# Optimization experiments

Measured on AMD Instinct MI355X. Metric: run time of the kernel, lower is better.

## Reference

```python
import jax, jax.numpy as jnp
import numpy as np

N, E, IN, H, OUT, G = 50000, 800000, 128, 256, 10, 512


def setup_inputs() -> dict:
    key = jax.random.key(0)
    ks = jax.random.split(key, 12)
    def lin(k, fan_in, fan_out):
        s = 1.0 / np.sqrt(fan_in)
        kw, kb = jax.random.split(k)
        W = jax.random.uniform(kw, (fan_in, fan_out), jnp.float32, -s, s)
        b = jax.random.uniform(kb, (fan_out,), jnp.float32, -s, s)
        return W, b
    x = jax.random.normal(ks[0], (N, IN), jnp.float32)
    edge_index = jax.random.randint(ks[1], (2, E), 0, N)
    batch = jnp.sort(jax.random.randint(ks[2], (N,), 0, G))
    W1a, b1a = lin(ks[3], IN, H)
    W1b, b1b = lin(ks[4], H, H)
    W2a, b2a = lin(ks[5], H, H)
    W2b, b2b = lin(ks[6], H, H)
    Wlin, blin = lin(ks[7], H, OUT)
    eps1 = jnp.zeros((), jnp.float32)
    eps2 = jnp.zeros((), jnp.float32)
    return dict(x=x, edge_index=edge_index, batch=batch,
                eps1=eps1, W1a=W1a, b1a=b1a, W1b=W1b, b1b=b1b,
                eps2=eps2, W2a=W2a, b2a=b2a, W2b=W2b, b2b=b2b,
                Wlin=Wlin, blin=blin)


def reference(x, edge_index, batch, eps1, W1a, b1a, W1b, b1b,
              eps2, W2a, b2a, W2b, b2b, Wlin, blin):
    src, dst = edge_index[0], edge_index[1]
    # GINConv 1: h = MLP((1+eps)*x + sum_{j in N(i)} x_j)
    agg = jax.ops.segment_sum(x[src], dst, num_segments=N)  # [N, IN]
    h = (1.0 + eps1) * x + agg
    h = jax.nn.relu(h @ W1a + b1a) @ W1b + b1b              # [N, H]
    h = jax.nn.relu(h)  # (dropout p=0.3 is identity in eval mode)
    # GINConv 2
    agg2 = jax.ops.segment_sum(h[src], dst, num_segments=N)  # [N, H]
    h2 = (1.0 + eps2) * h + agg2
    h2 = jax.nn.relu(h2 @ W2a + b2a) @ W2b + b2b             # [N, H]
    # global mean pool per graph
    psum = jax.ops.segment_sum(h2, batch, num_segments=G)    # [G, H]
    cnt = jax.ops.segment_sum(jnp.ones((N, 1), h2.dtype), batch, num_segments=G)
    pooled = psum / jnp.maximum(cnt, 1.0)
    out = pooled @ Wlin + blin                               # [G, OUT]
    return jax.nn.log_softmax(out, axis=-1)
```

## Files before the change

kernel.cpp:

```cpp
#include <hip/hip_runtime.h>
#include <math.h>
#include <stdint.h>

constexpr int N   = 50000;
constexpr int E   = 800000;
constexpr int IN  = 128;
constexpr int H   = 256;
constexpr int OUT = 10;
constexpr int G   = 512;
constexpr int BSTR = 64;

constexpr int NPART  = 391;
constexpr int SEGCAP = 48;
constexpr int EPB    = 4096;
constexpr int AB     = (E + EPB - 1) / EPB;

typedef __bf16 bf16x8 __attribute__((ext_vector_type(8)));
typedef float  f32x4  __attribute__((ext_vector_type(4)));
typedef float  f32x2  __attribute__((ext_vector_type(2)));

__device__ __forceinline__ float blo(unsigned v) { return __uint_as_float(v << 16); }
__device__ __forceinline__ float bhi(unsigned v) { return __uint_as_float(v & 0xffff0000u); }
__device__ __forceinline__ unsigned short f2b(float f) {
  unsigned u = __float_as_uint(f);
  u += 0x7fffu + ((u >> 16) & 1u);
  return (unsigned short)(u >> 16);
}
__device__ __forceinline__ unsigned packb(float lo, float hi) {
  return (unsigned)f2b(lo) | ((unsigned)f2b(hi) << 16);
}
__device__ __forceinline__ unsigned pk_fp8x4(float a, float b, float c, float d) {
  int r = 0;
  r = __builtin_amdgcn_cvt_pk_fp8_f32(a, b, r, false);
  r = __builtin_amdgcn_cvt_pk_fp8_f32(c, d, r, true);
  return (unsigned)r;
}
__device__ __forceinline__ unsigned char fp8_1(float v) {
  return (unsigned char)(__builtin_amdgcn_cvt_pk_fp8_f32(v, v, 0, false) & 0xff);
}


constexpr int XQ_BLOCKS  = (N * IN / 4) / 256;
constexpr int W1A_BLOCKS = (256 * IN) / 256;
constexpr int WH_BLOCKS  = (256 * H) / 256;

__global__ __launch_bounds__(256) void prep_kernel(
    const int* __restrict__ srcp, const int* __restrict__ dstp,
    unsigned* __restrict__ pbuf, int* __restrict__ pcnt,
    const float* __restrict__ x, unsigned* __restrict__ xq,
    const float* __restrict__ W1a, unsigned short* __restrict__ Wt1a,
    const float* __restrict__ W1b, unsigned short* __restrict__ Wt1b,
    const float* __restrict__ W2a, unsigned short* __restrict__ Wt2a,
    const float* __restrict__ W2b, unsigned short* __restrict__ Wt2b) {
  __shared__ int lcur[NPART];
  int b = blockIdx.x;
  int t = threadIdx.x;
  if (b < AB) {
    for (int j = t; j < NPART; j += 256) lcur[j] = 0;
    __syncthreads();
    const int e0 = b * EPB;
#pragma unroll
    for (int r = 0; r < EPB / 1024; ++r) {
      int base = e0 + (r * 256 + t) * 4;
      if (base < E) {
        int4 d4 = *(const int4*)(dstp + base);
        int4 s4 = *(const int4*)(srcp + base);
        int dd[4] = {d4.x, d4.y, d4.z, d4.w};
        int ss[4] = {s4.x, s4.y, s4.z, s4.w};
#pragma unroll
        for (int u = 0; u < 4; ++u) {
          int part = dd[u] >> 7, dl = dd[u] & 127;
          int pos = atomicAdd(&lcur[part], 1);
          if (pos < SEGCAP)
            pbuf[((size_t)part * AB + b) * SEGCAP + pos] =
                ((unsigned)dl << 16) | (unsigned)ss[u];
        }
      }
    }
    __syncthreads();
    for (int j = t; j < NPART; j += 256) pcnt[b * NPART + j] = min(lcur[j], SEGCAP);
    return;
  }
  b -= AB;
  if (b < XQ_BLOCKS) {
    int id = b * 256 + t;
    float4 v = ((const float4*)x)[id];
    xq[id] = pk_fp8x4(v.x, v.y, v.z, v.w);
    return;
  }
  b -= XQ_BLOCKS;
  if (b < W1A_BLOCKS) {
    int id = b * 256 + t;
    int n = id >> 7, k = id & 127;
    Wt1a[id] = f2b(W1a[k * 256 + n]);
    return;
  }
  b -= W1A_BLOCKS;
  const float* Ws;
  unsigned short* Wd;
  if (b < WH_BLOCKS)            { Ws = W1b; Wd = Wt1b; }
  else if (b < 2 * WH_BLOCKS)   { Ws = W2a; Wd = Wt2a; b -= WH_BLOCKS; }
  else                          { Ws = W2b; Wd = Wt2b; b -= 2 * WH_BLOCKS; }
  int id = b * 256 + t;
  int n = id >> 8, k = id & 255;
  Wd[id] = f2b(Ws[k * 256 + n]);
}


__global__ __launch_bounds__(256) void csr_kernel(const unsigned* __restrict__ pbuf,
                                                  const int* __restrict__ pcnt,
                                                  int* __restrict__ deg, int* __restrict__ csre) {
  __shared__ int sa[256], sb[256];
  __shared__ int ldeg[128];
  int p = blockIdx.x;
  int t = threadIdx.x;
  if (t < 128) ldeg[t] = 0;
  sa[t] = (t < AB) ? pcnt[t * NPART + p] : 0;
  __syncthreads();
  int* cur = sa; int* nxt = sb;
#pragma unroll
  for (int off = 1; off < 256; off <<= 1) {
    nxt[t] = cur[t] + ((t >= off) ? cur[t - off] : 0);
    __syncthreads();
    int* tmp = cur; cur = nxt; nxt = tmp;
  }
  int T = cur[255];
  const unsigned* seg = pbuf + (size_t)p * AB * SEGCAP;
  for (int f = t; f < T; f += 256) {
    int lo = 0, hi = AB - 1;
    while (lo < hi) { int m = (lo + hi) >> 1; if (cur[m] > f) hi = m; else lo = m + 1; }
    int bb = lo;
    int excl = bb ? cur[bb - 1] : 0;
    unsigned v = seg[(size_t)bb * SEGCAP + (f - excl)];
    int dl = (int)(v >> 16), s = (int)(v & 0xFFFFu);
    int pos = atomicAdd(&ldeg[dl], 1);
    if (pos < BSTR) csre[(((size_t)p << 7) + dl) * BSTR + pos] = s;
  }
  __syncthreads();
  if (t < 128) {
    int node = (p << 7) + t;
    if (node < N) deg[node] = min(ldeg[t], BSTR);
  }
}


template <int RS>
__global__ __launch_bounds__(64) void agg_pair_kernel(
    const unsigned char* __restrict__ inq,
    const int* __restrict__ deg, const int* __restrict__ csre,
    const float* __restrict__ epsp, unsigned short* __restrict__ out) {
  constexpr int NPAIR = N / 2;
  int bx = blockIdx.x;
  int half = (RS == 256) ? (bx / NPAIR) : 0;
  int pair = (RS == 256) ? (bx - half * NPAIR) : bx;
  int lane = threadIdx.x;
  int hsel = lane >> 5;
  int l = lane & 31;
  int i = pair * 2 + hsel;
  int dg = deg[i]; if (dg > BSTR) dg = BSTR;
  const int* bkt = csre + (size_t)i * BSTR;
  int dgmax = max(dg, __shfl_xor(dg, 32));
  const unsigned char* rowbase = inq + half * 128 + l * 4;
  float a0 = 0.f, a1 = 0.f, a2 = 0.f, a3 = 0.f;
  int hi_j = dg - 1; if (hi_j < 0) hi_j = 0;
  for (int j = 0; j < dgmax; j += 8) {
    unsigned idx[8], v[8];
#pragma unroll
    for (int u = 0; u < 8; ++u) {
      int jc = j + u; if (jc > hi_j) jc = hi_j;
      unsigned raw = (unsigned)bkt[jc];
      idx[u] = raw < (unsigned)N ? raw : 0u;
    }
#pragma unroll
    for (int u = 0; u < 8; ++u) v[u] = *(const unsigned*)(rowbase + (size_t)idx[u] * RS);
#pragma unroll
    for (int u = 0; u < 8; ++u) {
      float s = (j + u < dg) ? 1.f : 0.f;
      f32x2 lo = __builtin_amdgcn_cvt_pk_f32_fp8((int)v[u], false);
      f32x2 hh = __builtin_amdgcn_cvt_pk_f32_fp8((int)v[u], true);
      a0 += s * lo.x; a1 += s * lo.y; a2 += s * hh.x; a3 += s * hh.y;
    }
  }
  float sc = 1.0f + epsp[0];
  unsigned sv = *(const unsigned*)(rowbase + (size_t)i * RS);
  f32x2 slo = __builtin_amdgcn_cvt_pk_f32_fp8((int)sv, false);
  f32x2 shi = __builtin_amdgcn_cvt_pk_f32_fp8((int)sv, true);
  a0 += sc * slo.x; a1 += sc * slo.y; a2 += sc * shi.x; a3 += sc * shi.y;
  unsigned short* orow = out + (size_t)i * RS + half * 128 + l * 4;
  *(uint2*)orow = make_uint2(packb(a0, a1), packb(a2, a3));
}


template <int K, bool RELU, bool OUT8>
__global__ __launch_bounds__(256, 2) void gemm_bf16_kernel(const unsigned short* __restrict__ A,
                                                           const unsigned short* __restrict__ Bt,
                                                           const float* __restrict__ bias,
                                                           void* __restrict__ outv,
                                                           int Nrows) {
  constexpr int M = 256, LDK = 40;
  __shared__ __align__(16) unsigned short As[128 * LDK];
  __shared__ __align__(16) unsigned short Bs[256 * LDK];
  const int tid  = threadIdx.x;
  const int r0   = blockIdx.x * 128;
  const int wave = tid >> 6, lane = tid & 63;
  const int quad = lane >> 4, l15 = lane & 15;
  const int wrow = (wave >> 1) * 64, wcol = (wave & 1) * 64;
  const int srow = tid >> 2;
  const int sk8  = (tid & 3) * 8;

  f32x4 acc[2][4][4];
#pragma unroll
  for (int c = 0; c < 2; ++c)
#pragma unroll
    for (int i = 0; i < 4; ++i)
#pragma unroll
      for (int j = 0; j < 4; ++j) acc[c][i][j] = (f32x4){0.f, 0.f, 0.f, 0.f};

  for (int k0 = 0; k0 < K; k0 += 32) {
    {
      int grow = r0 + srow;
      uint4 v = make_uint4(0u, 0u, 0u, 0u);
      if (grow < Nrows) v = *(const uint4*)(A + (size_t)grow * K + k0 + sk8);
      *(uint4*)(As + srow * LDK + sk8) = v;
      grow = r0 + srow + 64;
      uint4 w = make_uint4(0u, 0u, 0u, 0u);
      if (grow < Nrows) w = *(const uint4*)(A + (size_t)grow * K + k0 + sk8);
      *(uint4*)(As + (srow + 64) * LDK + sk8) = w;
#pragma unroll
      for (int sgm = 0; sgm < 4; ++sgm) {
        int col = srow + sgm * 64;
        *(uint4*)(Bs + col * LDK + sk8) = *(const uint4*)(Bt + (size_t)col * K + k0 + sk8);
      }
    }
    __syncthreads();
    bf16x8 af[4];
#pragma unroll
    for (int mt = 0; mt < 4; ++mt)
      af[mt] = *(const bf16x8*)(As + (wrow + mt * 16 + l15) * LDK + quad * 8);
#pragma unroll
    for (int ch = 0; ch < 2; ++ch) {
      bf16x8 bfr[4];
#pragma unroll
      for (int nt = 0; nt < 4; ++nt)
        bfr[nt] = *(const bf16x8*)(Bs + (ch * 128 + wcol + nt * 16 + l15) * LDK + quad * 8);
#pragma unroll
      for (int mt = 0; mt < 4; ++mt)
#pragma unroll
        for (int nt = 0; nt < 4; ++nt)
          acc[ch][mt][nt] =
              __builtin_amdgcn_mfma_f32_16x16x32_bf16(af[mt], bfr[nt], acc[ch][mt][nt], 0, 0, 0);
    }
    __syncthreads();
  }

#pragma unroll
  for (int ch = 0; ch < 2; ++ch) {
    float bv[4];
#pragma unroll
    for (int nt = 0; nt < 4; ++nt) bv[nt] = bias[ch * 128 + wcol + nt * 16 + l15];
#pragma unroll
    for (int mt = 0; mt < 4; ++mt) {
      int gr0 = r0 + wrow + mt * 16 + quad * 4;
#pragma unroll
      for (int i = 0; i < 4; ++i) {
        int grow = gr0 + i;
        if (grow >= Nrows) continue;
#pragma unroll
        for (int nt = 0; nt < 4; ++nt) {
          float v = acc[ch][mt][nt][i] + bv[nt];
          if (RELU) v = fmaxf(v, 0.f);
          int col = ch * 128 + wcol + nt * 16 + l15;
          if (OUT8) ((unsigned char*)outv)[(size_t)grow * M + col] = fp8_1(v);
          else      ((unsigned short*)outv)[(size_t)grow * M + col] = f2b(v);
        }
      }
    }
  }
}


__global__ __launch_bounds__(128) void pool_final_kernel(const unsigned short* __restrict__ h2,
                                                         const int* __restrict__ batch,
                                                         const float* __restrict__ Wlin,
                                                         const float* __restrict__ blin,
                                                         float* __restrict__ out) {
  __shared__ float sp[H];
  __shared__ float logits[OUT];
  int g = blockIdx.x;
  int t = threadIdx.x;
  int lo = 0, hi = N;
  while (lo < hi) { int m = (lo + hi) >> 1; if (batch[m] < g) lo = m + 1; else hi = m; }
  int s = lo;
  lo = 0; hi = N;
  while (lo < hi) { int m = (lo + hi) >> 1; if (batch[m] < g + 1) lo = m + 1; else hi = m; }
  int e = lo;
  float a0 = 0.f, a1 = 0.f;
  const unsigned* base = (const unsigned*)h2;
  int n = s;
  for (; n + 4 <= e; n += 4) {
    unsigned v0 = base[(size_t)(n + 0) * (H / 2) + t];
    unsigned v1 = base[(size_t)(n + 1) * (H / 2) + t];
    unsigned v2 = base[(size_t)(n + 2) * (H / 2) + t];
    unsigned v3 = base[(size_t)(n + 3) * (H / 2) + t];
    a0 += blo(v0) + blo(v1) + blo(v2) + blo(v3);
    a1 += bhi(v0) + bhi(v1) + bhi(v2) + bhi(v3);
  }
  for (; n < e; ++n) {
    unsigned v = base[(size_t)n * (H / 2) + t];
    a0 += blo(v); a1 += bhi(v);
  }
  float inv = 1.0f / fmaxf((float)(e - s), 1.0f);
  sp[2 * t]     = a0 * inv;
  sp[2 * t + 1] = a1 * inv;
  __syncthreads();
  if (t < OUT) {
    float acc = blin[t];
    for (int k = 0; k < H; ++k) acc = fmaf(sp[k], Wlin[k * OUT + t], acc);
    logits[t] = acc;
  }
  __syncthreads();
  if (t == 0) {
    float m = -INFINITY;
    for (int j = 0; j < OUT; ++j) m = fmaxf(m, logits[j]);
    float ssum = 0.f;
    for (int j = 0; j < OUT; ++j) ssum += expf(logits[j] - m);
    float ls = logf(ssum);
    for (int j = 0; j < OUT; ++j) out[(size_t)g * OUT + j] = logits[j] - m - ls;
  }
}


static inline char* align_up(char* p, size_t a) {
  return (char*)(((uintptr_t)p + a - 1) & ~(a - 1));
}

extern "C" void kernel_launch(void* const* d_in, const int* in_sizes, int n_in,
                              void* d_out, int out_size, void* d_ws, size_t ws_size,
                              hipStream_t stream) {
  const float* x    = (const float*)d_in[0];
  const int*   ei   = (const int*)d_in[1];
  const int*   srcp = ei;
  const int*   dstp = ei + E;
  const int*   batch = (const int*)d_in[2];
  const float* eps1 = (const float*)d_in[3];
  const float* W1a  = (const float*)d_in[4];
  const float* b1a  = (const float*)d_in[5];
  const float* W1b  = (const float*)d_in[6];
  const float* b1b  = (const float*)d_in[7];
  const float* eps2 = (const float*)d_in[8];
  const float* W2a  = (const float*)d_in[9];
  const float* b2a  = (const float*)d_in[10];
  const float* W2b  = (const float*)d_in[11];
  const float* b2b  = (const float*)d_in[12];
  const float* Wlin = (const float*)d_in[13];
  const float* blin = (const float*)d_in[14];
  float* outp = (float*)d_out;

  char* p = (char*)d_ws;
  unsigned* pbuf = (unsigned*)p;     p = align_up(p + (size_t)NPART * AB * SEGCAP * 4, 256);
  int* pcnt = (int*)p;               p = align_up(p + (size_t)AB * NPART * 4, 256);
  int* deg  = (int*)p;               p = align_up(p + (size_t)N * 4, 256);
  int* csre = (int*)p;               p = align_up(p + (size_t)NPART * 128 * BSTR * 4, 256);
  unsigned* xq = (unsigned*)p;       p = align_up(p + (size_t)N * IN, 256);
  unsigned char* h1q = (unsigned char*)p;  p = align_up(p + (size_t)N * H, 256);
  unsigned short* B1 = (unsigned short*)p; p = align_up(p + (size_t)N * IN * 2, 256);
  unsigned short* B2 = (unsigned short*)p; p = align_up(p + (size_t)N * H * 2, 256);
  unsigned short* B3 = (unsigned short*)p; p = align_up(p + (size_t)N * H * 2, 256);
  unsigned short* Wt1a = (unsigned short*)p;  p = align_up(p + (size_t)H * IN * 2, 256);
  unsigned short* Wt1b = (unsigned short*)p;  p = align_up(p + (size_t)H * H * 2, 256);
  unsigned short* Wt2a = (unsigned short*)p;  p = align_up(p + (size_t)H * H * 2, 256);
  unsigned short* Wt2b = (unsigned short*)p;  p = align_up(p + (size_t)H * H * 2, 256);

  prep_kernel<<<AB + XQ_BLOCKS + W1A_BLOCKS + 3 * WH_BLOCKS, 256, 0, stream>>>(
      srcp, dstp, pbuf, pcnt, x, xq, W1a, Wt1a, W1b, Wt1b, W2a, Wt2a, W2b, Wt2b);

  csr_kernel<<<NPART, 256, 0, stream>>>(pbuf, pcnt, deg, csre);

  const int ggrid = (N + 127) / 128;

  agg_pair_kernel<IN><<<N / 2, 64, 0, stream>>>((const unsigned char*)xq, deg, csre, eps1, B1);
  gemm_bf16_kernel<IN, true, false><<<ggrid, 256, 0, stream>>>(B1, Wt1a, b1a, B2, N);
  gemm_bf16_kernel<H, true, true><<<ggrid, 256, 0, stream>>>(B2, Wt1b, b1b, h1q, N);

  agg_pair_kernel<H><<<N, 64, 0, stream>>>(h1q, deg, csre, eps2, B3);
  gemm_bf16_kernel<H, true, false><<<ggrid, 256, 0, stream>>>(B3, Wt2a, b2a, B2, N);
  gemm_bf16_kernel<H, false, false><<<ggrid, 256, 0, stream>>>(B2, Wt2b, b2b, B3, N);

  pool_final_kernel<<<G, 128, 0, stream>>>(B3, batch, Wlin, blin, outp);
}
```

Measured before the change: 262.5 us.

## Fuse both MLP layers of each GIN conv into one GEMM kernel

Result: faster. 256.9 us (-2.2%).

```diff
diff --git a/kernel.cpp b/kernel.cpp
--- a/kernel.cpp
+++ b/kernel.cpp
@@ -37,6 +37,9 @@
 }
 __device__ __forceinline__ unsigned char fp8_1(float v) {
   return (unsigned char)(__builtin_amdgcn_cvt_pk_fp8_f32(v, v, 0, false) & 0xff);
+}
+__device__ __forceinline__ f32x2 upk_fp8(unsigned short s) {
+  return __builtin_amdgcn_cvt_pk_f32_fp8((int)s, false);
 }
 
 
@@ -191,15 +194,19 @@
 }
 
 
-template <int K, bool RELU, bool OUT8>
-__global__ __launch_bounds__(256, 2) void gemm_bf16_kernel(const unsigned short* __restrict__ A,
-                                                           const unsigned short* __restrict__ Bt,
-                                                           const float* __restrict__ bias,
-                                                           void* __restrict__ outv,
-                                                           int Nrows) {
-  constexpr int M = 256, LDK = 40;
-  __shared__ __align__(16) unsigned short As[128 * LDK];
-  __shared__ __align__(16) unsigned short Bs[256 * LDK];
+template <int K1, bool RELU2, bool OUT8>
+__global__ __launch_bounds__(256, 2) void mlp_kernel(
+    const unsigned short* __restrict__ A,
+    const unsigned short* __restrict__ Bta,
+    const float* __restrict__ ba,
+    const unsigned short* __restrict__ Btb,
+    const float* __restrict__ bb,
+    void* __restrict__ outv, int Nrows) {
+  constexpr int M = 256, LDK = 40, LDI = 168;
+  __shared__ __align__(16) unsigned short sh[10240 + 21504];
+  unsigned short* Bs = sh;
+  unsigned short* Is = sh + 10240;
+  unsigned short* As = sh + 10240;
   const int tid  = threadIdx.x;
   const int r0   = blockIdx.x * 128;
   const int wave = tid >> 6, lane = tid & 63;
@@ -208,28 +215,28 @@
   const int srow = tid >> 2;
   const int sk8  = (tid & 3) * 8;
 
-  f32x4 acc[2][4][4];
+  f32x4 acc1[2][4][4];
 #pragma unroll
   for (int c = 0; c < 2; ++c)
 #pragma unroll
     for (int i = 0; i < 4; ++i)
 #pragma unroll
-      for (int j = 0; j < 4; ++j) acc[c][i][j] = (f32x4){0.f, 0.f, 0.f, 0.f};
-
-  for (int k0 = 0; k0 < K; k0 += 32) {
+      for (int j = 0; j < 4; ++j) acc1[c][i][j] = (f32x4){0.f, 0.f, 0.f, 0.f};
+
+  for (int k0 = 0; k0 < K1; k0 += 32) {
     {
       int grow = r0 + srow;
       uint4 v = make_uint4(0u, 0u, 0u, 0u);
-      if (grow < Nrows) v = *(const uint4*)(A + (size_t)grow * K + k0 + sk8);
+      if (grow < Nrows) v = *(const uint4*)(A + (size_t)grow * K1 + k0 + sk8);
       *(uint4*)(As + srow * LDK + sk8) = v;
       grow = r0 + srow + 64;
       uint4 w = make_uint4(0u, 0u, 0u, 0u);
-      if (grow < Nrows) w = *(const uint4*)(A + (size_t)grow * K + k0 + sk8);
+      if (grow < Nrows) w = *(const uint4*)(A + (size_t)grow * K1 + k0 + sk8);
       *(uint4*)(As + (srow + 64) * LDK + sk8) = w;
 #pragma unroll
       for (int sgm = 0; sgm < 4; ++sgm) {
         int col = srow + sgm * 64;
-        *(uint4*)(Bs + col * LDK + sk8) = *(const uint4*)(Bt + (size_t)col * K + k0 + sk8);
+        *(uint4*)(Bs + col * LDK + sk8) = *(const uint4*)(Bta + (size_t)col * K1 + k0 + sk8);
       }
     }
     __syncthreads();
@@ -247,17 +254,75 @@
       for (int mt = 0; mt < 4; ++mt)
 #pragma unroll
         for (int nt = 0; nt < 4; ++nt)
-          acc[ch][mt][nt] =
-              __builtin_amdgcn_mfma_f32_16x16x32_bf16(af[mt], bfr[nt], acc[ch][mt][nt], 0, 0, 0);
-    }
-    __syncthreads();
-  }
-
-#pragma unroll
+          acc1[ch][mt][nt] =
+              __builtin_amdgcn_mfma_f32_16x16x32_bf16(af[mt], bfr[nt], acc1[ch][mt][nt], 0, 0, 0);
+    }
+    __syncthreads();
+  }
+
+  float bva[2][4];
+#pragma unroll
+  for (int c = 0; c < 2; ++c)
+#pragma unroll
+    for (int nt = 0; nt < 4; ++nt) bva[c][nt] = ba[c * 128 + wcol + nt * 16 + l15];
+
+  f32x4 acc2[2][4][4];
+#pragma unroll
+  for (int c = 0; c < 2; ++c)
+#pragma unroll
+    for (int i = 0; i < 4; ++i)
+#pragma unroll
+      for (int j = 0; j < 4; ++j) acc2[c][i][j] = (f32x4){0.f, 0.f, 0.f, 0.f};
+
   for (int ch = 0; ch < 2; ++ch) {
+    __syncthreads();
+#pragma unroll
+    for (int mt = 0; mt < 4; ++mt)
+#pragma unroll
+      for (int nt = 0; nt < 4; ++nt) {
+        int col = wcol + nt * 16 + l15;
+        int rbase = wrow + mt * 16 + quad * 4;
+#pragma unroll
+        for (int i = 0; i < 4; ++i)
+          Is[(rbase + i) * LDI + col] = f2b(fmaxf(acc1[ch][mt][nt][i] + bva[ch][nt], 0.f));
+      }
+    for (int kk = 0; kk < 4; ++kk) {
+      __syncthreads();
+      {
+        int k0 = ch * 128 + kk * 32;
+#pragma unroll
+        for (int sgm = 0; sgm < 4; ++sgm) {
+          int col = srow + sgm * 64;
+          *(uint4*)(Bs + col * LDK + sk8) = *(const uint4*)(Btb + (size_t)col * 256 + k0 + sk8);
+        }
+      }
+      __syncthreads();
+      bf16x8 af[4];
+#pragma unroll
+      for (int mt = 0; mt < 4; ++mt)
+        af[mt] = *(const bf16x8*)(Is + (wrow + mt * 16 + l15) * LDI + kk * 32 + quad * 8);
+#pragma unroll
+      for (int c2 = 0; c2 < 2; ++c2) {
+        bf16x8 bfr[4];
+#pragma unroll
+        for (int nt = 0; nt < 4; ++nt)
+          bfr[nt] = *(const bf16x8*)(Bs + (c2 * 128 + wcol + nt * 16 + l15) * LDK + quad * 8);
+#pragma unroll
+        for (int mt = 0; mt < 4; ++mt)
+#pragma unroll
+          for (int nt = 0; nt < 4; ++nt)
+            acc2[c2][mt][nt] =
+                __builtin_amdgcn_mfma_f32_16x16x32_bf16(af[mt], bfr[nt], acc2[c2][mt][nt], 0, 0, 0);
+      }
+    }
+    __syncthreads();
+  }
+
+#pragma unroll
+  for (int c2 = 0; c2 < 2; ++c2) {
     float bv[4];
 #pragma unroll
-    for (int nt = 0; nt < 4; ++nt) bv[nt] = bias[ch * 128 + wcol + nt * 16 + l15];
+    for (int nt = 0; nt < 4; ++nt) bv[nt] = bb[c2 * 128 + wcol + nt * 16 + l15];
 #pragma unroll
     for (int mt = 0; mt < 4; ++mt) {
       int gr0 = r0 + wrow + mt * 16 + quad * 4;
@@ -267,9 +332,9 @@
         if (grow >= Nrows) continue;
 #pragma unroll
         for (int nt = 0; nt < 4; ++nt) {
-          float v = acc[ch][mt][nt][i] + bv[nt];
-          if (RELU) v = fmaxf(v, 0.f);
-          int col = ch * 128 + wcol + nt * 16 + l15;
+          float v = acc2[c2][mt][nt][i] + bv[nt];
+          if (RELU2) v = fmaxf(v, 0.f);
+          int col = c2 * 128 + wcol + nt * 16 + l15;
           if (OUT8) ((unsigned char*)outv)[(size_t)grow * M + col] = fp8_1(v);
           else      ((unsigned short*)outv)[(size_t)grow * M + col] = f2b(v);
         }
@@ -379,12 +444,10 @@
   const int ggrid = (N + 127) / 128;
 
   agg_pair_kernel<IN><<<N / 2, 64, 0, stream>>>((const unsigned char*)xq, deg, csre, eps1, B1);
-  gemm_bf16_kernel<IN, true, false><<<ggrid, 256, 0, stream>>>(B1, Wt1a, b1a, B2, N);
-  gemm_bf16_kernel<H, true, true><<<ggrid, 256, 0, stream>>>(B2, Wt1b, b1b, h1q, N);
+  mlp_kernel<IN, true, true><<<ggrid, 256, 0, stream>>>(B1, Wt1a, b1a, Wt1b, b1b, h1q, N);
 
   agg_pair_kernel<H><<<N, 64, 0, stream>>>(h1q, deg, csre, eps2, B3);
-  gemm_bf16_kernel<H, true, false><<<ggrid, 256, 0, stream>>>(B3, Wt2a, b2a, B2, N);
-  gemm_bf16_kernel<H, false, false><<<ggrid, 256, 0, stream>>>(B2, Wt2b, b2b, B3, N);
-
-  pool_final_kernel<<<G, 128, 0, stream>>>(B3, batch, Wlin, blin, outp);
-}
+  mlp_kernel<H, false, false><<<ggrid, 256, 0, stream>>>(B3, Wt2a, b2a, Wt2b, b2b, B2, N);
+
+  pool_final_kernel<<<G, 128, 0, stream>>>(B2, batch, Wlin, blin, outp);
+}
```
